# Kernel tuning notes

Hardware: AMD Instinct MI355X
Metric: run time of the kernel (lower is better)

Reference implementation:

```python
import jax, jax.numpy as jnp
import numpy as np

B, S, D = 2, 2048, 1024
H, Hd = 16, 64
THD = H * Hd  # total_head_dim
LAMBDA_INIT = 0.8
ROPE_BASE = 10000.0
GN_EPS = 1e-5


def _rope_tables(seq_len, head_dim, dtype):
    inv_freq = 1.0 / (ROPE_BASE ** (jnp.arange(0, head_dim, 2, dtype=jnp.float32) / head_dim))
    t = jnp.arange(seq_len, dtype=jnp.float32)
    freqs = jnp.outer(t, inv_freq)                      # (S, Hd/2)
    emb = jnp.concatenate([freqs, freqs], axis=-1)      # (S, Hd)
    return jnp.cos(emb).astype(dtype), jnp.sin(emb).astype(dtype)


def _rotate_half(x):
    x1, x2 = jnp.split(x, 2, axis=-1)
    return jnp.concatenate([-x2, x1], axis=-1)


def _apply_rope(q, k, cos, sin):
    # q, k: (B, H, S, Hd); cos/sin: (S, Hd)
    cos = cos[None, None, :, :]
    sin = sin[None, None, :, :]
    q = q * cos + _rotate_half(q) * sin
    k = k * cos + _rotate_half(k) * sin
    return q, k


def setup_inputs() -> dict:
    key = jax.random.key(0)
    ks = jax.random.split(key, 8)
    s_in = 1.0 / np.sqrt(D)
    s_out = 1.0 / np.sqrt(THD)
    return {
        "x": jax.random.normal(ks[0], (B, S, D), dtype=jnp.float32),
        "Wq": jax.random.normal(ks[1], (D, 2 * THD), dtype=jnp.float32) * s_in,
        "Wk": jax.random.normal(ks[2], (D, 2 * THD), dtype=jnp.float32) * s_in,
        "Wv": jax.random.normal(ks[3], (D, THD), dtype=jnp.float32) * s_in,
        "Wo": jax.random.normal(ks[4], (THD, D), dtype=jnp.float32) * s_out,
        "lambda_q1": jnp.full((H,), LAMBDA_INIT, dtype=jnp.float32),
        "lambda_k1": jnp.full((H,), LAMBDA_INIT, dtype=jnp.float32),
        "lambda_q2": jnp.full((H,), LAMBDA_INIT, dtype=jnp.float32),
        "lambda_k2": jnp.full((H,), LAMBDA_INIT, dtype=jnp.float32),
        "lambda_init": jnp.asarray(LAMBDA_INIT, dtype=jnp.float32),
        "gn_weight": jnp.ones((THD,), dtype=jnp.float32),
        "gn_bias": jnp.zeros((THD,), dtype=jnp.float32),
    }


def reference(x, Wq, Wk, Wv, Wo, lambda_q1, lambda_k1, lambda_q2, lambda_k2,
              lambda_init, gn_weight, gn_bias):
    b, s, _ = x.shape
    scale = Hd ** -0.5

    q = (x @ Wq).reshape(b, s, 2, H, Hd).transpose(0, 2, 3, 1, 4)  # (B,2,H,S,Hd)
    k = (x @ Wk).reshape(b, s, 2, H, Hd).transpose(0, 2, 3, 1, 4)
    v = (x @ Wv).reshape(b, s, H, Hd).transpose(0, 2, 1, 3)        # (B,H,S,Hd)

    q1, q2 = q[:, 0], q[:, 1]
    k1, k2 = k[:, 0], k[:, 1]

    cos, sin = _rope_tables(s, Hd, x.dtype)
    q1, k1 = _apply_rope(q1, k1, cos, sin)
    q2, k2 = _apply_rope(q2, k2, cos, sin)

    attn1 = jax.nn.softmax(jnp.einsum("bhqd,bhkd->bhqk", q1, k1) * scale, axis=-1)
    attn2 = jax.nn.softmax(jnp.einsum("bhqd,bhkd->bhqk", q2, k2) * scale, axis=-1)

    lam1 = jnp.exp(lambda_q1 * lambda_k1).reshape(1, H, 1, 1)
    lam2 = jnp.exp(lambda_q2 * lambda_k2).reshape(1, H, 1, 1)
    lam_full = lam1 - lam2 + lambda_init

    attn_diff = attn1 - lam_full * attn2
    out = jnp.einsum("bhqk,bhkd->bhqd", attn_diff, v)              # (B,H,S,Hd)
    out = out.transpose(0, 2, 1, 3).reshape(b * s, H, Hd)           # (B*S,H,Hd)

    # GroupNorm with num_groups=H over channels THD: normalize each head's Hd
    mean = out.mean(axis=-1, keepdims=True)
    var = out.var(axis=-1, keepdims=True)
    out = (out - mean) * jax.lax.rsqrt(var + GN_EPS)
    out = out * gn_weight.reshape(H, Hd) + gn_bias.reshape(H, Hd)

    out = out.reshape(b, s, THD) * (1.0 - lambda_init)
    return out @ Wo
```

## Files before the change

### kernel.cpp

```cpp
#include <hip/hip_runtime.h>
#include <hip/hip_fp16.h>
#include <math.h>

#define NH     16
#define HD     64
#define S_LEN  2048
#define THD_   1024
#define SCALE_LOG2E 0.18033688011112042f

typedef __fp16 f16x8 __attribute__((ext_vector_type(8)));
typedef __fp16 f16x4 __attribute__((ext_vector_type(4)));
typedef __fp16 f16x2 __attribute__((ext_vector_type(2)));
typedef float  f32x4 __attribute__((ext_vector_type(4)));


__device__ inline void wt_body(const float* __restrict__ W,
                               __half* __restrict__ WT, int id, int nmask,
                               int nshift) {
  int n = id & nmask;
  int k8 = (id >> nshift) * 8;
  int N = nmask + 1;
  f16x8 h;
#pragma unroll
  for (int j = 0; j < 8; ++j)
    h[j] = (__fp16)W[(size_t)(k8 + j) * N + n];
  *(f16x8*)(WT + (size_t)n * 1024 + k8) = h;
}

__global__ __launch_bounds__(256) void prep_kernel(
    const float* __restrict__ Wq, const float* __restrict__ Wk,
    __half* __restrict__ WqT, __half* __restrict__ WkT,
    float2* __restrict__ tab) {
  int bid = blockIdx.x;
  int t = threadIdx.x;
  if (bid < 1024) {
    wt_body(Wq, WqT, bid * 256 + t, 2047, 11);
  } else if (bid < 2048) {
    wt_body(Wk, WkT, (bid - 1024) * 256 + t, 2047, 11);
  } else {
    int id = (bid - 2048) * 256 + t;
    int p = id & 31;
    int s = id >> 5;
    float inv = expf(-0.28782313662425574f * (float)p);
    float sn, cs;
    sincosf((float)s * inv, &sn, &cs);
    tab[id] = make_float2(cs, sn);
  }
}

template <int MODE>
__global__ __launch_bounds__(256) void mfma_gemm(const void* __restrict__ Ap,
                                                 const void* __restrict__ Bp,
                                                 void* __restrict__ Cp,
                                                 const float2* __restrict__ tab) {
  __shared__ __fp16 As[128][72];
  __shared__ __fp16 Bs[64][72];
  const int t = threadIdx.x;
  const int w = t >> 6, lane = t & 63;
  const int quad = lane >> 4, lqi = lane & 15;
  const int wm = w * 32;
  const int n0 = blockIdx.x * 64, m0 = blockIdx.y * 128;

  f32x4 acc[2][4];
#pragma unroll
  for (int mt = 0; mt < 2; ++mt)
#pragma unroll
    for (int nt = 0; nt < 4; ++nt) acc[mt][nt] = (f32x4){0.f, 0.f, 0.f, 0.f};

  const int srow = t >> 3;
  const int sc8 = (t & 7) * 8;
  const int gn_ = t & 63;
  const int gk0 = (t >> 6) * 8;

  for (int k0 = 0; k0 < 1024; k0 += 64) {
    if (k0) __syncthreads();
    if (MODE == 3) {
      const __half* A16 = (const __half*)Ap;
#pragma unroll
      for (int p = 0; p < 4; ++p) {
        int row = srow + 32 * p;
        *(f16x8*)&As[row][sc8] =
            *(const f16x8*)(A16 + (size_t)(m0 + row) * 1024 + k0 + sc8);
      }
    } else {
      const float* A32 = (const float*)Ap;
#pragma unroll
      for (int p = 0; p < 4; ++p) {
        int row = srow + 32 * p;
        const float* src = A32 + (size_t)(m0 + row) * 1024 + k0 + sc8;
        float4 u = *(const float4*)src;
        float4 v = *(const float4*)(src + 4);
        f16x8 h;
        h[0] = (__fp16)u.x; h[1] = (__fp16)u.y;
        h[2] = (__fp16)u.z; h[3] = (__fp16)u.w;
        h[4] = (__fp16)v.x; h[5] = (__fp16)v.y;
        h[6] = (__fp16)v.z; h[7] = (__fp16)v.w;
        *(f16x8*)&As[row][sc8] = h;
      }
    }
    if (MODE == 2) {
      const float* B32 = (const float*)Bp;
#pragma unroll
      for (int p = 0; p < 2; ++p) {
        int kc = gk0 + 32 * p;
        f16x8 h;
#pragma unroll
        for (int j = 0; j < 8; ++j)
          h[j] = (__fp16)B32[(size_t)(k0 + kc + j) * 1024 + n0 + gn_];
        *(f16x8*)&Bs[gn_][kc] = h;
      }
    } else {
      const __half* B16 = (const __half*)Bp;
      if (srow < 32) {
#pragma unroll
        for (int p = 0; p < 2; ++p) {
          int row = srow + 32 * p;
          *(f16x8*)&Bs[row][sc8] =
              *(const f16x8*)(B16 + (size_t)(n0 + row) * 1024 + k0 + sc8);
        }
      }
    }
    __syncthreads();
#pragma unroll
    for (int ks = 0; ks < 2; ++ks) {
      f16x8 af[2], bf[4];
#pragma unroll
      for (int mt = 0; mt < 2; ++mt)
        af[mt] = *(const f16x8*)&As[wm + mt * 16 + lqi][ks * 32 + quad * 8];
#pragma unroll
      for (int nt = 0; nt < 4; ++nt)
        bf[nt] = *(const f16x8*)&Bs[nt * 16 + lqi][ks * 32 + quad * 8];
#pragma unroll
      for (int mt = 0; mt < 2; ++mt)
#pragma unroll
        for (int nt = 0; nt < 4; ++nt)
          acc[mt][nt] = __builtin_amdgcn_mfma_f32_16x16x32_f16(
              af[mt], bf[nt], acc[mt][nt], 0, 0, 0);
    }
  }

  const int b = m0 >> 11;
  const int s0 = (m0 & 2047) + wm + quad * 4;
  if (MODE == 0 || MODE == 1) {
    __half* dst = (__half*)Cp;
    const int comp = n0 >> 10, hh = (n0 >> 6) & 15;
    __half* base = dst + ((size_t)(b * 2 + comp) * NH + hh) * (size_t)S_LEN * HD;
#pragma unroll
    for (int nt = 0; nt < 2; ++nt) {
      int p = nt * 16 + lqi;
#pragma unroll
      for (int mt = 0; mt < 2; ++mt) {
#pragma unroll
        for (int i = 0; i < 4; ++i) {
          int s = s0 + mt * 16 + i;
          float2 cs = tab[s * 32 + p];
          float x1 = acc[mt][nt][i], x2 = acc[mt][nt + 2][i];
          float y1 = x1 * cs.x - x2 * cs.y;
          float y2 = x2 * cs.x + x1 * cs.y;
          if (MODE == 1) { y1 *= SCALE_LOG2E; y2 *= SCALE_LOG2E; }
          base[(size_t)s * HD + p] = __float2half(y1);
          base[(size_t)s * HD + p + 32] = __float2half(y2);
        }
      }
    }
  } else if (MODE == 2) {
    __half* vt = (__half*)Cp;
    const int hh = n0 >> 6;
#pragma unroll
    for (int nt = 0; nt < 4; ++nt) {
      int hd = nt * 16 + lqi;
      __half* base = vt + (((size_t)b * NH + hh) * HD + hd) * S_LEN;
#pragma unroll
      for (int mt = 0; mt < 2; ++mt) {
        f16x4 hv;
#pragma unroll
        for (int i = 0; i < 4; ++i) hv[i] = (__fp16)acc[mt][nt][i];
        *(f16x4*)(base + s0 + mt * 16) = hv;
      }
    }
  } else {
    float* Co = (float*)Cp;
#pragma unroll
    for (int mt = 0; mt < 2; ++mt)
#pragma unroll
      for (int i = 0; i < 4; ++i) {
        int m = m0 + wm + mt * 16 + quad * 4 + i;
#pragma unroll
        for (int nt = 0; nt < 4; ++nt)
          Co[(size_t)m * 1024 + n0 + nt * 16 + lqi] = acc[mt][nt][i];
      }
  }
}

__global__ __launch_bounds__(256, 2) void attn_kernel(
    const __half* __restrict__ q_h, const __half* __restrict__ k_h,
    const __half* __restrict__ vt_h, float* __restrict__ out,
    const float* __restrict__ lq1, const float* __restrict__ lk1,
    const float* __restrict__ lq2, const float* __restrict__ lk2,
    const float* __restrict__ lam_init_p) {
  __shared__ __half Ks[2][16][512];
  __shared__ __half Vs[2][64][64];

  const int t = threadIdx.x;
  const int w = t >> 6, lane = t & 63;
  const int quad = lane >> 4, lqi = lane & 15;
  const int r7 = lane & 7;
  const int qt = blockIdx.x;
  const int bh = blockIdx.y;
  const int b = bh >> 4, h = bh & 15;

  const size_t c1 = ((size_t)(b * 2 + 0) * NH + h) * (size_t)S_LEN * HD;
  const size_t c2 = ((size_t)(b * 2 + 1) * NH + h) * (size_t)S_LEN * HD;
  const size_t vtb = ((size_t)b * NH + h) * (size_t)HD * S_LEN;
  const int q0 = qt * 128 + w * 32;

  f16x8 qf[2][2][2];
#pragma unroll
  for (int nt = 0; nt < 2; ++nt)
#pragma unroll
    for (int ks = 0; ks < 2; ++ks) {
      size_t a = (size_t)(q0 + nt * 16 + lqi) * HD + ks * 32 + quad * 8;
      qf[0][nt][ks] = *(const f16x8*)(q_h + c1 + a);
      qf[1][nt][ks] = *(const f16x8*)(q_h + c2 + a);
    }

  f32x4 O[2][4][2];
#pragma unroll
  for (int s = 0; s < 2; ++s)
#pragma unroll
    for (int hm = 0; hm < 4; ++hm)
#pragma unroll
      for (int nt = 0; nt < 2; ++nt) O[s][hm][nt] = (f32x4){0.f, 0.f, 0.f, 0.f};
  float lsum[2][2] = {{0.f, 0.f}, {0.f, 0.f}};

  auto stage = [&](int c, int k0, int buf) {
    const __half* src;
    __half* dst;
    if (c < 16) {
      int str = c >> 3, mt = (c >> 1) & 3, ks = c & 1;
      src = k_h + (str ? c2 : c1) + (size_t)(k0 + mt * 16 + lqi) * HD +
            ks * 32 + quad * 8;
      dst = &Ks[buf][c][0];
    } else {
      int cc = c - 16;
      src = vt_h + vtb + (size_t)(cc * 8 + (lane >> 3)) * S_LEN + k0 +
            ((lane & 7) ^ (lane >> 3)) * 8;
      dst = &Vs[buf][cc * 8][0];
    }
    __builtin_amdgcn_global_load_lds(
        (const __attribute__((address_space(1))) unsigned int*)(const void*)src,
        (__attribute__((address_space(3))) unsigned int*)(void*)dst, 16, 0, 0);
  };

#pragma unroll
  for (int ci = 0; ci < 6; ++ci) stage(w + ci * 4, 0, 0);
  __syncthreads();

  for (int kt = 0; kt < 32; ++kt) {
    const int cur = kt & 1;
    if (kt < 31) {
#pragma unroll
      for (int ci = 0; ci < 6; ++ci) stage(w + ci * 4, (kt + 1) * 64, cur ^ 1);
    }

#pragma unroll
    for (int g = 0; g < 2; ++g) {
      f16x8 vf[4];
#pragma unroll
      for (int hm = 0; hm < 4; ++hm) {
        const __half* vrow = &Vs[cur][hm * 16 + lqi][0];
        int s0 = (g * 4 + (quad >> 1)) ^ r7;
        int s1 = (g * 4 + 2 + (quad >> 1)) ^ r7;
        union { f16x8 v8; f16x4 v4[2]; } u;
        u.v4[0] = *(const f16x4*)(vrow + s0 * 8 + (quad & 1) * 4);
        u.v4[1] = *(const f16x4*)(vrow + s1 * 8 + (quad & 1) * 4);
        vf[hm] = u.v8;
      }
      f16x8 bfrag[2][2];
#pragma unroll
      for (int str = 0; str < 2; ++str) {
        f16x8 kf00 = *(const f16x8*)&Ks[cur][str * 8 + g * 4 + 0][lane * 8];
        f16x8 kf01 = *(const f16x8*)&Ks[cur][str * 8 + g * 4 + 1][lane * 8];
        f16x8 kf10 = *(const f16x8*)&Ks[cur][str * 8 + g * 4 + 2][lane * 8];
        f16x8 kf11 = *(const f16x8*)&Ks[cur][str * 8 + g * 4 + 3][lane * 8];
#pragma unroll
        for (int nt = 0; nt < 2; ++nt) {
          f32x4 sa = (f32x4){0.f, 0.f, 0.f, 0.f};
          f32x4 sb = (f32x4){0.f, 0.f, 0.f, 0.f};
          sa = __builtin_amdgcn_mfma_f32_16x16x32_f16(kf00, qf[str][nt][0], sa,
                                                      0, 0, 0);
          sa = __builtin_amdgcn_mfma_f32_16x16x32_f16(kf01, qf[str][nt][1], sa,
                                                      0, 0, 0);
          sb = __builtin_amdgcn_mfma_f32_16x16x32_f16(kf10, qf[str][nt][0], sb,
                                                      0, 0, 0);
          sb = __builtin_amdgcn_mfma_f32_16x16x32_f16(kf11, qf[str][nt][1], sb,
                                                      0, 0, 0);
          float ea0 = __builtin_amdgcn_exp2f(sa[0]);
          float ea1 = __builtin_amdgcn_exp2f(sa[1]);
          float ea2 = __builtin_amdgcn_exp2f(sa[2]);
          float ea3 = __builtin_amdgcn_exp2f(sa[3]);
          float eb0 = __builtin_amdgcn_exp2f(sb[0]);
          float eb1 = __builtin_amdgcn_exp2f(sb[1]);
          float eb2 = __builtin_amdgcn_exp2f(sb[2]);
          float eb3 = __builtin_amdgcn_exp2f(sb[3]);
          lsum[str][nt] += ((ea0 + ea1) + (ea2 + ea3)) +
                           ((eb0 + eb1) + (eb2 + eb3));
          union { f16x8 v; f16x2 h2[4]; } pu;
          pu.h2[0] = __builtin_amdgcn_cvt_pkrtz(ea0, ea1);
          pu.h2[1] = __builtin_amdgcn_cvt_pkrtz(ea2, ea3);
          pu.h2[2] = __builtin_amdgcn_cvt_pkrtz(eb0, eb1);
          pu.h2[3] = __builtin_amdgcn_cvt_pkrtz(eb2, eb3);
          bfrag[str][nt] = pu.v;
        }
      }
#pragma unroll
      for (int hm = 0; hm < 4; ++hm)
#pragma unroll
        for (int str = 0; str < 2; ++str)
#pragma unroll
          for (int nt = 0; nt < 2; ++nt)
            O[str][hm][nt] = __builtin_amdgcn_mfma_f32_16x16x32_f16(
                vf[hm], bfrag[str][nt], O[str][hm][nt], 0, 0, 0);
    }

    if (kt < 31) __syncthreads();
  }

  const float lam0 = lam_init_p[0];
  const float lam = expf(lq1[h] * lk1[h]) - expf(lq2[h] * lk2[h]) + lam0;
#pragma unroll
  for (int str = 0; str < 2; ++str)
#pragma unroll
    for (int nt = 0; nt < 2; ++nt) {
      float v = lsum[str][nt];
      v += __shfl_xor(v, 16);
      v += __shfl_xor(v, 32);
      lsum[str][nt] = v;
    }
#pragma unroll
  for (int nt = 0; nt < 2; ++nt) {
    float il1 = 1.f / lsum[0][nt];
    float il2 = lam / lsum[1][nt];
    int q = q0 + nt * 16 + lqi;
#pragma unroll
    for (int hm = 0; hm < 4; ++hm) {
      f32x4 o;
#pragma unroll
      for (int i = 0; i < 4; ++i)
        o[i] = O[0][hm][nt][i] * il1 - O[1][hm][nt][i] * il2;
      *(f32x4*)(out + ((size_t)(b * S_LEN + q)) * THD_ + h * HD + hm * 16 +
                quad * 4) = o;
    }
  }
}

__global__ __launch_bounds__(256) void gn_wt_kernel(
    const float* __restrict__ src, __half* __restrict__ dst,
    const float* __restrict__ gw, const float* __restrict__ gb,
    const float* __restrict__ lam_init_p, const float* __restrict__ Wo,
    __half* __restrict__ WoT) {
  if (blockIdx.x >= 16384) {
    wt_body(Wo, WoT, (blockIdx.x - 16384) * 256 + threadIdx.x, 1023, 10);
    return;
  }
  int g = blockIdx.x * 4 + (threadIdx.x >> 6);
  int lane = threadIdx.x & 63;
  float v = src[(size_t)g * 64 + lane];
  float s = v, sq = v * v;
#pragma unroll
  for (int off = 32; off; off >>= 1) {
    s += __shfl_xor(s, off);
    sq += __shfl_xor(sq, off);
  }
  float mean = s * (1.f / 64.f);
  float var = sq * (1.f / 64.f) - mean * mean;
  float rs = rsqrtf(var + 1e-5f);
  int h = g & 15;
  float w = gw[h * 64 + lane], bb = gb[h * 64 + lane];
  dst[(size_t)g * 64 + lane] =
      __float2half(((v - mean) * rs * w + bb) * (1.f - lam_init_p[0]));
}

extern "C" void kernel_launch(void* const* d_in, const int* in_sizes, int n_in,
                              void* d_out, int out_size, void* d_ws,
                              size_t ws_size, hipStream_t stream) {
  const float* x = (const float*)d_in[0];
  const float* Wq = (const float*)d_in[1];
  const float* Wk = (const float*)d_in[2];
  const float* Wv = (const float*)d_in[3];
  const float* Wo = (const float*)d_in[4];
  const float* lq1 = (const float*)d_in[5];
  const float* lk1 = (const float*)d_in[6];
  const float* lq2 = (const float*)d_in[7];
  const float* lk2 = (const float*)d_in[8];
  const float* lam_init = (const float*)d_in[9];
  const float* gnw = (const float*)d_in[10];
  const float* gnb = (const float*)d_in[11];
  float* out = (float*)d_out;

  __half* q_h = (__half*)d_ws;
  __half* k_h = q_h + 8388608;
  __half* vt_h = k_h + 8388608;
  __half* WqT = k_h;
  __half* WkT = vt_h;
  float2* tab = (float2*)(vt_h + 2097152);
  __half* WoT = q_h;
  __half* gn_h = q_h + 1048576;

  dim3 blk(256);
  prep_kernel<<<2304, blk, 0, stream>>>(Wq, Wk, WqT, WkT, tab);
  mfma_gemm<1><<<dim3(32, 32), blk, 0, stream>>>(x, WqT, q_h, tab);
  mfma_gemm<0><<<dim3(32, 32), blk, 0, stream>>>(x, WkT, k_h, tab);
  mfma_gemm<2><<<dim3(16, 32), blk, 0, stream>>>(x, Wv, vt_h, nullptr);
  attn_kernel<<<dim3(16, 32), blk, 0, stream>>>(q_h, k_h, vt_h, out, lq1, lk1,
                                                lq2, lk2, lam_init);
  gn_wt_kernel<<<16896, blk, 0, stream>>>(out, gn_h, gnw, gnb, lam_init, Wo,
                                          WoT);
  mfma_gemm<3><<<dim3(16, 32), blk, 0, stream>>>(gn_h, WoT, out, nullptr);
}
```

Baseline: 319.4 us.

## Stage GEMM tiles via direct global-to-LDS loads in fragment-major layout

The projection GEMM now fills shared memory with global_load_lds DMA instead of staging through registers. A and B tiles are laid out fragment-major so each lane reads its MFMA fragment contiguously. For fp32 A inputs, the raw floats are kept in LDS and converted to fp16 at fragment-read time, which doubles A's LDS footprint to 32KB. The aim is to cut register-staged load/convert/store work and LDS bank conflicts, at the cost of more LDS per block and repeated conversions inside the inner loop.

After: 408.6 us. 27.9% more time.

```diff
diff --git a/kernel.cpp b/kernel.cpp
--- a/kernel.cpp
+++ b/kernel.cpp
@@ -12,6 +12,11 @@
 typedef __fp16 f16x4 __attribute__((ext_vector_type(4)));
 typedef __fp16 f16x2 __attribute__((ext_vector_type(2)));
 typedef float  f32x4 __attribute__((ext_vector_type(4)));
+
+#define GLDS16(src, dst)                                                      \
+  __builtin_amdgcn_global_load_lds(                                           \
+      (const __attribute__((address_space(1))) unsigned int*)(const void*)(src), \
+      (__attribute__((address_space(3))) unsigned int*)(void*)(dst), 16, 0, 0)
 
 
 __device__ inline void wt_body(const float* __restrict__ W,
@@ -53,12 +58,16 @@
                                                  const void* __restrict__ Bp,
                                                  void* __restrict__ Cp,
                                                  const float2* __restrict__ tab) {
-  __shared__ __fp16 As[128][72];
-  __shared__ __fp16 Bs[64][72];
+  __shared__ __attribute__((aligned(16))) char AsRaw[32768];
+  __shared__ __half Bs[4][2][64][8];
+  typedef float  AFrag32[2][2][64][4];
+  typedef __half AFrag16[2][64][8];
+  AFrag32* As32 = (AFrag32*)AsRaw;
+  AFrag16* As16 = (AFrag16*)AsRaw;
+
   const int t = threadIdx.x;
   const int w = t >> 6, lane = t & 63;
   const int quad = lane >> 4, lqi = lane & 15;
-  const int wm = w * 32;
   const int n0 = blockIdx.x * 64, m0 = blockIdx.y * 128;
 
   f32x4 acc[2][4];
@@ -67,8 +76,6 @@
 #pragma unroll
     for (int nt = 0; nt < 4; ++nt) acc[mt][nt] = (f32x4){0.f, 0.f, 0.f, 0.f};
 
-  const int srow = t >> 3;
-  const int sc8 = (t & 7) * 8;
   const int gn_ = t & 63;
   const int gk0 = (t >> 6) * 8;
 
@@ -76,47 +83,57 @@
     if (k0) __syncthreads();
     if (MODE == 3) {
       const __half* A16 = (const __half*)Ap;
-#pragma unroll
-      for (int p = 0; p < 4; ++p) {
-        int row = srow + 32 * p;
-        *(f16x8*)&As[row][sc8] =
-            *(const f16x8*)(A16 + (size_t)(m0 + row) * 1024 + k0 + sc8);
+      const __half* B16 = (const __half*)Bp;
+#pragma unroll
+      for (int ci = 0; ci < 6; ++ci) {
+        int c = w + ci * 4;
+        if (c < 16) {
+          int mt2 = c >> 1, ks = c & 1;
+          GLDS16(A16 + (size_t)(m0 + mt2 * 16 + lqi) * 1024 + k0 + ks * 32 +
+                     quad * 8,
+                 &As16[mt2][ks][0][0]);
+        } else {
+          int cc = c - 16, nt2 = cc >> 1, ks = cc & 1;
+          GLDS16(B16 + (size_t)(n0 + nt2 * 16 + lqi) * 1024 + k0 + ks * 32 +
+                     quad * 8,
+                 &Bs[nt2][ks][0][0]);
+        }
+      }
+    } else if (MODE == 2) {
+      const float* A32 = (const float*)Ap;
+#pragma unroll
+      for (int ci = 0; ci < 8; ++ci) {
+        int c = w + ci * 4;
+        int mt2 = c >> 2, ks = (c >> 1) & 1, half = c & 1;
+        GLDS16(A32 + (size_t)(m0 + mt2 * 16 + lqi) * 1024 + k0 + ks * 32 +
+                   quad * 8 + half * 4,
+               &As32[mt2][ks][half][0][0]);
+      }
+      const float* B32 = (const float*)Bp;
+#pragma unroll
+      for (int p = 0; p < 2; ++p) {
+        f16x8 h;
+#pragma unroll
+        for (int j = 0; j < 8; ++j)
+          h[j] = (__fp16)B32[(size_t)(k0 + p * 32 + gk0 + j) * 1024 + n0 + gn_];
+        *(f16x8*)&Bs[gn_ >> 4][p][w * 16 + (gn_ & 15)][0] = h;
       }
     } else {
       const float* A32 = (const float*)Ap;
-#pragma unroll
-      for (int p = 0; p < 4; ++p) {
-        int row = srow + 32 * p;
-        const float* src = A32 + (size_t)(m0 + row) * 1024 + k0 + sc8;
-        float4 u = *(const float4*)src;
-        float4 v = *(const float4*)(src + 4);
-        f16x8 h;
-        h[0] = (__fp16)u.x; h[1] = (__fp16)u.y;
-        h[2] = (__fp16)u.z; h[3] = (__fp16)u.w;
-        h[4] = (__fp16)v.x; h[5] = (__fp16)v.y;
-        h[6] = (__fp16)v.z; h[7] = (__fp16)v.w;
-        *(f16x8*)&As[row][sc8] = h;
-      }
-    }
-    if (MODE == 2) {
-      const float* B32 = (const float*)Bp;
-#pragma unroll
-      for (int p = 0; p < 2; ++p) {
-        int kc = gk0 + 32 * p;
-        f16x8 h;
-#pragma unroll
-        for (int j = 0; j < 8; ++j)
-          h[j] = (__fp16)B32[(size_t)(k0 + kc + j) * 1024 + n0 + gn_];
-        *(f16x8*)&Bs[gn_][kc] = h;
-      }
-    } else {
       const __half* B16 = (const __half*)Bp;
-      if (srow < 32) {
-#pragma unroll
-        for (int p = 0; p < 2; ++p) {
-          int row = srow + 32 * p;
-          *(f16x8*)&Bs[row][sc8] =
-              *(const f16x8*)(B16 + (size_t)(n0 + row) * 1024 + k0 + sc8);
+#pragma unroll
+      for (int ci = 0; ci < 10; ++ci) {
+        int c = w + ci * 4;
+        if (c < 32) {
+          int mt2 = c >> 2, ks = (c >> 1) & 1, half = c & 1;
+          GLDS16(A32 + (size_t)(m0 + mt2 * 16 + lqi) * 1024 + k0 + ks * 32 +
+                     quad * 8 + half * 4,
+                 &As32[mt2][ks][half][0][0]);
+        } else {
+          int cc = c - 32, nt2 = cc >> 1, ks = cc & 1;
+          GLDS16(B16 + (size_t)(n0 + nt2 * 16 + lqi) * 1024 + k0 + ks * 32 +
+                     quad * 8,
+                 &Bs[nt2][ks][0][0]);
         }
       }
     }
@@ -125,11 +142,23 @@
     for (int ks = 0; ks < 2; ++ks) {
       f16x8 af[2], bf[4];
 #pragma unroll
-      for (int mt = 0; mt < 2; ++mt)
-        af[mt] = *(const f16x8*)&As[wm + mt * 16 + lqi][ks * 32 + quad * 8];
+      for (int mt = 0; mt < 2; ++mt) {
+        if (MODE == 3) {
+          af[mt] = *(const f16x8*)&As16[w * 2 + mt][ks][lane][0];
+        } else {
+          f32x4 lo = *(const f32x4*)&As32[w * 2 + mt][ks][0][lane][0];
+          f32x4 hi = *(const f32x4*)&As32[w * 2 + mt][ks][1][lane][0];
+          f16x8 h;
+          h[0] = (__fp16)lo[0]; h[1] = (__fp16)lo[1];
+          h[2] = (__fp16)lo[2]; h[3] = (__fp16)lo[3];
+          h[4] = (__fp16)hi[0]; h[5] = (__fp16)hi[1];
+          h[6] = (__fp16)hi[2]; h[7] = (__fp16)hi[3];
+          af[mt] = h;
+        }
+      }
 #pragma unroll
       for (int nt = 0; nt < 4; ++nt)
-        bf[nt] = *(const f16x8*)&Bs[nt * 16 + lqi][ks * 32 + quad * 8];
+        bf[nt] = *(const f16x8*)&Bs[nt][ks][lane][0];
 #pragma unroll
       for (int mt = 0; mt < 2; ++mt)
 #pragma unroll
@@ -140,6 +169,7 @@
   }
 
   const int b = m0 >> 11;
+  const int wm = w * 32;
   const int s0 = (m0 & 2047) + wm + quad * 4;
   if (MODE == 0 || MODE == 1) {
     __half* dst = (__half*)Cp;
@@ -247,9 +277,7 @@
             ((lane & 7) ^ (lane >> 3)) * 8;
       dst = &Vs[buf][cc * 8][0];
     }
-    __builtin_amdgcn_global_load_lds(
-        (const __attribute__((address_space(1))) unsigned int*)(const void*)src,
-        (__attribute__((address_space(3))) unsigned int*)(void*)dst, 16, 0, 0);
+    GLDS16(src, dst);
   };
 
 #pragma unroll
```
